# Performance work log

Measured on AMD Instinct MI355X. Metric: run time of the kernel, lower is better.

Reference implementation:

```python
import jax, jax.numpy as jnp
import numpy as np

L = 3          # num_layers
D = 512        # hidden_dim
B, N = 8, 1024
EPS = 1e-5


def layernorm(x, gamma, beta):
    mu = jnp.mean(x, axis=-1, keepdims=True)
    var = jnp.var(x, axis=-1, keepdims=True)
    return (x - mu) * jax.lax.rsqrt(var + EPS) * gamma + beta


def setup_inputs() -> dict:
    key = jax.random.key(0)
    ks = jax.random.split(key, 12)
    s = 1.0 / np.sqrt(D)
    node_features = jax.random.normal(ks[0], (B, N, D), dtype=jnp.float32)
    adjacency_matrix = jax.random.randint(ks[1], (B, N, N), 0, 2, dtype=jnp.int32)
    return {
        "node_features": node_features,
        "adjacency_matrix": adjacency_matrix,
        # attn_linear: Linear(2D, 1) -> weight [2D], bias scalar, per layer
        "attn_w": jax.random.normal(ks[2], (L, 2 * D), dtype=jnp.float32) * (1.0 / np.sqrt(2 * D)),
        "attn_b": jax.random.normal(ks[3], (L,), dtype=jnp.float32) * 0.01,
        "W1": jax.random.normal(ks[4], (L, D, 4 * D), dtype=jnp.float32) * s,
        "b1": jnp.zeros((L, 4 * D), dtype=jnp.float32),
        "W2": jax.random.normal(ks[5], (L, 4 * D, D), dtype=jnp.float32) * (1.0 / np.sqrt(4 * D)),
        "b2": jnp.zeros((L, D), dtype=jnp.float32),
        "g1": jnp.ones((L, D), dtype=jnp.float32),
        "beta1": jnp.zeros((L, D), dtype=jnp.float32),
        "g2": jnp.ones((L, D), dtype=jnp.float32),
        "beta2": jnp.zeros((L, D), dtype=jnp.float32),
    }


def reference(node_features, adjacency_matrix, attn_w, attn_b, W1, b1, W2, b2, g1, beta1, g2, beta2):
    n = adjacency_matrix.shape[-1]
    # adjacency + self loops; mask of allowed edges
    mask = (adjacency_matrix.astype(jnp.float32) + jnp.eye(n, dtype=jnp.float32)) > 0  # [B,N,N]
    x = node_features
    d = x.shape[-1]
    for l in range(attn_w.shape[0]):
        # score_ij = a1.h_i + a2.h_j + b  (== Linear(concat(h_i,h_j)))
        si = x @ attn_w[l, :d]           # [B,N]
        sj = x @ attn_w[l, d:]           # [B,N]
        scores = si[:, :, None] + sj[:, None, :] + attn_b[l]   # [B,N,N]
        scores = jnp.where(scores >= 0, scores, 0.2 * scores)  # LeakyReLU(0.2)
        scores = jnp.where(mask, scores, -jnp.inf)
        attn = jax.nn.softmax(scores, axis=-1)                  # diag always unmasked
        agg = jnp.einsum('bij,bjd->bid', attn, x)
        h = layernorm(x + agg, g1[l], beta1[l])
        ff = jax.nn.gelu(h @ W1[l] + b1[l], approximate=False) @ W2[l] + b2[l]
        x = layernorm(h + ff, g2[l], beta2[l])
    return x
```

## Files before the change

kernel.cpp:

```cpp
#include <hip/hip_runtime.h>
#include <math.h>

#define NB 8
#define NN 1024
#define DD 512

typedef unsigned short u16;
typedef unsigned int u32;
typedef unsigned long long u64;
typedef __attribute__((ext_vector_type(8))) short bfrag;
typedef __attribute__((ext_vector_type(4))) float ffrag;

__device__ __forceinline__ u16 f2b(float f) {
    union { float f; u32 u; } v; v.f = f;
    u32 r = v.u + 0x7fffu + ((v.u >> 16) & 1u);
    return (u16)(r >> 16);
}
__device__ __forceinline__ float b2f(u16 b) {
    union { u32 u; float f; } v; v.u = ((u32)b) << 16;
    return v.f;
}

__device__ __forceinline__ float gelu_cheap(float v) {
    float s = v * 0.70710678118654752f;
    float a = fabsf(s);
    float t = 1.0f / (1.0f + 0.3275911f * a);
    float p = ((((1.061405429f * t - 1.453152027f) * t + 1.421413741f) * t
                - 0.284496736f) * t + 0.254829592f) * t;
    float erfa = 1.0f - p * __expf(-a * a);
    float erfs = copysignf(erfa, s);
    return 0.5f * v * (1.0f + erfs);
}

__device__ __forceinline__ void gload_lds16(const void* g, void* l) {
    __builtin_amdgcn_global_load_lds(
        (const __attribute__((address_space(1))) void*)g,
        (__attribute__((address_space(3))) void*)l, 16, 0, 0);
}

__global__ __launch_bounds__(256) void mask_pack(const int* __restrict__ adj,
                                                 u64* __restrict__ mb) {
    int idx = blockIdx.x * 256 + threadIdx.x;
    int w = idx & 15;
    int bi = idx >> 4;
    int i = bi & 1023;
    const int4* p = (const int4*)(adj + (size_t)bi * NN + w * 64);
    u64 m = 0;
#pragma unroll
    for (int q = 0; q < 16; ++q) {
        int4 v = p[q];
        if (v.x > 0) m |= 1ull << (q * 4 + 0);
        if (v.y > 0) m |= 1ull << (q * 4 + 1);
        if (v.z > 0) m |= 1ull << (q * 4 + 2);
        if (v.w > 0) m |= 1ull << (q * 4 + 3);
    }
    if (w == (i >> 6)) m |= 1ull << (i & 63);
    mb[idx] = m;
}

__global__ __launch_bounds__(256) void transpose_cvt(
    const float* __restrict__ in, u16* __restrict__ out,
    int R, int C, size_t inStr, size_t outStr)
{
    __shared__ float tile[32][33];
    int z = blockIdx.z;
    int r0 = blockIdx.y * 32, c0 = blockIdx.x * 32;
    int t = threadIdx.x;
    int tr = t >> 3, tc = (t & 7) * 4;
    float4 v = *(const float4*)(in + inStr * z + (size_t)(r0 + tr) * C + c0 + tc);
    tile[tr][tc + 0] = v.x; tile[tr][tc + 1] = v.y;
    tile[tr][tc + 2] = v.z; tile[tr][tc + 3] = v.w;
    __syncthreads();
    u32 w0 = (u32)f2b(tile[tc + 0][tr]) | ((u32)f2b(tile[tc + 1][tr]) << 16);
    u32 w1 = (u32)f2b(tile[tc + 2][tr]) | ((u32)f2b(tile[tc + 3][tr]) << 16);
    uint2 wv; wv.x = w0; wv.y = w1;
    *(uint2*)(out + outStr * z + (size_t)(c0 + tr) * R + r0 + tc) = wv;
}

__global__ __launch_bounds__(256) void score_proj_kernel(
    const float* __restrict__ x, const float* __restrict__ w,
    float* __restrict__ si, float* __restrict__ sj)
{
    int wave = threadIdx.x >> 6;
    int lane = threadIdx.x & 63;
    int row = blockIdx.x * 4 + wave;
    const float4* xr = (const float4*)(x + (size_t)row * DD) + lane * 2;
    const float4* w1 = (const float4*)(w) + lane * 2;
    const float4* w2 = (const float4*)(w + DD) + lane * 2;
    float a = 0.f, b2 = 0.f;
#pragma unroll
    for (int c = 0; c < 2; ++c) {
        float4 xv = xr[c], wa = w1[c], wb = w2[c];
        a  += xv.x * wa.x + xv.y * wa.y + xv.z * wa.z + xv.w * wa.w;
        b2 += xv.x * wb.x + xv.y * wb.y + xv.z * wb.z + xv.w * wb.w;
    }
#pragma unroll
    for (int off = 32; off > 0; off >>= 1) {
        a  += __shfl_xor(a, off);
        b2 += __shfl_xor(b2, off);
    }
    if (lane == 0) { si[row] = a; sj[row] = b2; }
}

__global__ __launch_bounds__(256) void softmax_p(
    const float* __restrict__ si, const float* __restrict__ sj,
    const float* __restrict__ attn_b, const u64* __restrict__ mb,
    u16* __restrict__ P)
{
    __shared__ u16 sb[8 * NN];
    int b  = blockIdx.x >> 7;
    int i0 = (blockIdx.x & 127) * 8;
    int tid = threadIdx.x;
    int r = tid >> 5, l32 = tid & 31;
    int i = i0 + r;
    float bb = attn_b[0];
    float siv = si[b * NN + i];
    const float* sjb = sj + b * NN;
    const u64* mbr = mb + ((size_t)b * NN + i) * 16;

    float sv[32];
    float mx = -INFINITY;
#pragma unroll
    for (int q = 0; q < 32; ++q) {
        int j = q * 32 + l32;
        u64 w = mbr[q >> 1];
        int bit = ((q & 1) << 5) + l32;
        float s = siv + sjb[j] + bb;
        s = (s >= 0.f) ? s : 0.2f * s;
        s = ((w >> bit) & 1ull) ? s : -INFINITY;
        sv[q] = s;
        mx = fmaxf(mx, s);
    }
#pragma unroll
    for (int off = 16; off > 0; off >>= 1) mx = fmaxf(mx, __shfl_xor(mx, off, 32));
    float sum = 0.f;
#pragma unroll
    for (int q = 0; q < 32; ++q) {
        float p = __expf(sv[q] - mx);
        sv[q] = p;
        sum += p;
    }
#pragma unroll
    for (int off = 16; off > 0; off >>= 1) sum += __shfl_xor(sum, off, 32);
    float inv = 1.f / sum;
#pragma unroll
    for (int q = 0; q < 32; ++q)
        sb[r * NN + q * 32 + l32] = f2b(sv[q] * inv);
    __syncthreads();
    const uint4* src = (const uint4*)sb;
    uint4* dst = (uint4*)(P + ((size_t)b * NN + i0) * NN);
#pragma unroll
    for (int t = 0; t < 4; ++t) dst[t * 256 + tid] = src[t * 256 + tid];
}

template <int EPI>
__global__ __launch_bounds__(256) void gemm64(
    const u16* __restrict__ A, const u16* __restrict__ Bm,
    const float* __restrict__ bias, const void* __restrict__ res,
    void* __restrict__ Cout, int K, int N, int lda, int ldb,
    size_t aStr, size_t bStr, size_t cStr, size_t resStr)
{
    __shared__ __align__(16) u16 lds[24576];
    int z = blockIdx.z;
    int m0 = blockIdx.y * 64, n0 = blockIdx.x * 128;
    int tid = threadIdx.x;
    int lane = tid & 63, wv = tid >> 6;

    const u16* ag[2]; const u16* bg[4];
    u32 la[2], lb[4];
#pragma unroll
    for (int i = 0; i < 2; ++i) {
        int q = i * 256 + tid;
        int row = q >> 3, c = q & 7;
        ag[i] = A + aStr * z + (size_t)(m0 + row) * lda + (c ^ (row & 7)) * 8;
        la[i] = i * 2048 + wv * 512;
    }
#pragma unroll
    for (int i = 0; i < 4; ++i) {
        int q = i * 256 + tid;
        int row = q >> 3, c = q & 7;
        bg[i] = Bm + bStr * z + (size_t)(n0 + row) * ldb + (c ^ (row & 7)) * 8;
        lb[i] = 8192 + i * 2048 + wv * 512;
    }

    int mw = (wv >> 1) * 32, nw = (wv & 1) * 64;
    int lr = lane & 15, lq = lane >> 4;
    int sw = lr & 7;

    ffrag acc[2][4];
#pragma unroll
    for (int i = 0; i < 2; ++i)
#pragma unroll
        for (int j = 0; j < 4; ++j) acc[i][j] = (ffrag){0.f, 0.f, 0.f, 0.f};

#pragma unroll
    for (int i = 0; i < 2; ++i) gload_lds16(ag[i], &lds[la[i]]);
#pragma unroll
    for (int i = 0; i < 4; ++i) gload_lds16(bg[i], &lds[lb[i]]);

    for (int k0 = 0; k0 < K; k0 += 64) {
        int cur = (k0 >> 6) & 1;
        if (k0 + 64 < K) {
#pragma unroll
            for (int i = 0; i < 2; ++i)
                gload_lds16(ag[i] + k0 + 64, &lds[((cur ^ 1) << 12) + la[i]]);
#pragma unroll
            for (int i = 0; i < 4; ++i)
                gload_lds16(bg[i] + k0 + 64, &lds[((cur ^ 1) << 13) + lb[i]]);
            asm volatile("s_waitcnt vmcnt(6)" ::: "memory");
        } else {
            asm volatile("s_waitcnt vmcnt(0)" ::: "memory");
        }
        asm volatile("s_barrier" ::: "memory");

        const u16* Ab = &lds[cur << 12];
        const u16* Bb = &lds[8192 + (cur << 13)];
#pragma unroll
        for (int h = 0; h < 2; ++h) {
            bfrag af[2], bf[4];
#pragma unroll
            for (int i = 0; i < 2; ++i)
                af[i] = *(const bfrag*)&Ab[(mw + i * 16 + lr) * 64 + ((h * 4 + lq) ^ sw) * 8];
#pragma unroll
            for (int j = 0; j < 4; ++j)
                bf[j] = *(const bfrag*)&Bb[(nw + j * 16 + lr) * 64 + ((h * 4 + lq) ^ sw) * 8];
#pragma unroll
            for (int i = 0; i < 2; ++i)
#pragma unroll
                for (int j = 0; j < 4; ++j)
                    acc[i][j] = __builtin_amdgcn_mfma_f32_16x16x32_bf16(af[i], bf[j], acc[i][j], 0, 0, 0);
        }
        asm volatile("s_waitcnt lgkmcnt(0)\ns_barrier" ::: "memory");
    }

    float* Cf = (float*)Cout + cStr * z;
    u16*   Cb = (u16*)Cout + cStr * z;
    const float* resf = (const float*)res;
    const u16*   resb = (const u16*)res;
#pragma unroll
    for (int i = 0; i < 2; ++i) {
        int row = m0 + mw + i * 16 + lq * 4;
#pragma unroll
        for (int j = 0; j < 4; ++j) {
            int col = n0 + nw + j * 16 + lr;
            float bv = (EPI != 0) ? bias[col] : 0.f;
#pragma unroll
            for (int r = 0; r < 4; ++r) {
                float v = acc[i][j][r] + bv;
                size_t off = (size_t)(row + r) * N + col;
                if (EPI == 1) {
                    Cb[off] = f2b(gelu_cheap(v));
                } else if (EPI == 0) {
                    Cf[off] = v + resf[resStr * z + off];
                } else {
                    Cf[off] = v + b2f(resb[off]);
                }
            }
        }
    }
}

template <bool BF>
__global__ __launch_bounds__(256) void ln_kernel(
    const float* __restrict__ in, const float* __restrict__ g,
    const float* __restrict__ be, void* __restrict__ out)
{
    int row = blockIdx.x;
    int tid = threadIdx.x;
    const float2* rp = (const float2*)(in + (size_t)row * DD);
    float2 v = rp[tid];
    float s  = v.x + v.y;
    float ss = v.x * v.x + v.y * v.y;
#pragma unroll
    for (int off = 32; off > 0; off >>= 1) {
        s  += __shfl_xor(s, off);
        ss += __shfl_xor(ss, off);
    }
    __shared__ float sh[8];
    int wave = tid >> 6, lane = tid & 63;
    if (lane == 0) { sh[wave] = s; sh[4 + wave] = ss; }
    __syncthreads();
    float S  = sh[0] + sh[1] + sh[2] + sh[3];
    float SS = sh[4] + sh[5] + sh[6] + sh[7];
    float mean = S * (1.f / DD);
    float var  = SS * (1.f / DD) - mean * mean;
    var = fmaxf(var, 0.f);
    float rs = rsqrtf(var + 1e-5f);
    float2 gv = ((const float2*)g)[tid];
    float2 bv = ((const float2*)be)[tid];
    float ox = (v.x - mean) * rs * gv.x + bv.x;
    float oy = (v.y - mean) * rs * gv.y + bv.y;
    if (BF) {
        u32 w = (u32)f2b(ox) | ((u32)f2b(oy) << 16);
        ((u32*)out)[(size_t)row * (DD / 2) + tid] = w;
    } else {
        float2 o; o.x = ox; o.y = oy;
        ((float2*)out)[(size_t)row * (DD / 2) + tid] = o;
    }
}

__global__ __launch_bounds__(256) void ln2st(
    const float* __restrict__ in, const float* __restrict__ g,
    const float* __restrict__ be, const float* __restrict__ wnx,
    float* __restrict__ xout, u16* __restrict__ xT,
    float* __restrict__ si, float* __restrict__ sj)
{
    __shared__ u16 tt[512 * 36];
    int row0 = blockIdx.x * 32;
    int b    = row0 >> 10;
    int rloc = row0 & 1023;
    int tid  = threadIdx.x;
    int r = tid >> 3, l8 = tid & 7;
    int row = row0 + r;

    const float4* rp = (const float4*)(in + (size_t)row * DD + l8 * 64);
    float4 v[16];
    float s = 0.f, ss = 0.f;
#pragma unroll
    for (int c = 0; c < 16; ++c) {
        v[c] = rp[c];
        s  += v[c].x + v[c].y + v[c].z + v[c].w;
        ss += v[c].x * v[c].x + v[c].y * v[c].y + v[c].z * v[c].z + v[c].w * v[c].w;
    }
#pragma unroll
    for (int off = 1; off < 8; off <<= 1) {
        s  += __shfl_xor(s, off);
        ss += __shfl_xor(ss, off);
    }
    float mean = s * (1.f / DD);
    float var  = ss * (1.f / DD) - mean * mean;
    var = fmaxf(var, 0.f);
    float rs = rsqrtf(var + 1e-5f);

    float a = 0.f, b2 = 0.f;
    float4* op = (float4*)(xout + (size_t)row * DD + l8 * 64);
#pragma unroll
    for (int c = 0; c < 16; ++c) {
        float4 gv = ((const float4*)g)[l8 * 16 + c];
        float4 bv = ((const float4*)be)[l8 * 16 + c];
        float4 o;
        o.x = (v[c].x - mean) * rs * gv.x + bv.x;
        o.y = (v[c].y - mean) * rs * gv.y + bv.y;
        o.z = (v[c].z - mean) * rs * gv.z + bv.z;
        o.w = (v[c].w - mean) * rs * gv.w + bv.w;
        op[c] = o;
        float4 wa = ((const float4*)wnx)[l8 * 16 + c];
        float4 wb = ((const float4*)(wnx + DD))[l8 * 16 + c];
        a  += o.x * wa.x + o.y * wa.y + o.z * wa.z + o.w * wa.w;
        b2 += o.x * wb.x + o.y * wb.y + o.z * wb.z + o.w * wb.w;
        int d = l8 * 64 + c * 4;
        tt[(d + 0) * 36 + r] = f2b(o.x);
        tt[(d + 1) * 36 + r] = f2b(o.y);
        tt[(d + 2) * 36 + r] = f2b(o.z);
        tt[(d + 3) * 36 + r] = f2b(o.w);
    }
#pragma unroll
    for (int off = 1; off < 8; off <<= 1) {
        a  += __shfl_xor(a, off);
        b2 += __shfl_xor(b2, off);
    }
    if (l8 == 0) { si[row] = a; sj[row] = b2; }

    __syncthreads();
#pragma unroll
    for (int t = 0; t < 2; ++t) {
        int d = t * 256 + tid;
        const uint2* src = (const uint2*)&tt[d * 36];
        uint2* dst = (uint2*)(xT + ((size_t)b * DD + d) * NN + rloc);
#pragma unroll
        for (int k = 0; k < 4; ++k) dst[k] = src[k];
#pragma unroll
        for (int k = 4; k < 8; ++k) dst[k] = src[k];
    }
}

extern "C" void kernel_launch(void* const* d_in, const int* in_sizes, int n_in,
                              void* d_out, int out_size, void* d_ws, size_t ws_size,
                              hipStream_t stream) {
    const float* nf     = (const float*)d_in[0];
    const int*   adj    = (const int*)d_in[1];
    const float* attn_w = (const float*)d_in[2];
    const float* attn_b = (const float*)d_in[3];
    const float* W1     = (const float*)d_in[4];
    const float* b1     = (const float*)d_in[5];
    const float* W2     = (const float*)d_in[6];
    const float* b2     = (const float*)d_in[7];
    const float* g1     = (const float*)d_in[8];
    const float* be1    = (const float*)d_in[9];
    const float* g2     = (const float*)d_in[10];
    const float* be2    = (const float*)d_in[11];
    float* out = (float*)d_out;

    char* wsb = (char*)d_ws;
    float* x_cur = (float*)(wsb);
    u16*   h_bf  = (u16*)(wsb + 16777216);
    char*  scr   = wsb + 25165824;
    u16*   P     = (u16*)scr;
    float* hres  = (float*)(scr + 16777216);
    u16*   mid   = (u16*)scr;
    u16*   xT    = (u16*)(wsb + 58720256);
    u16*   W1t   = (u16*)(wsb + 67108864);
    u16*   W2t   = (u16*)(wsb + 73400320);
    u64*   mask  = (u64*)(wsb + 79691776);
    float* si    = (float*)(wsb + 80740352);
    float* sj    = (float*)(wsb + 80773120);

    mask_pack<<<512, 256, 0, stream>>>(adj, mask);
    transpose_cvt<<<dim3(64, 16, 3), 256, 0, stream>>>(W1, W1t, 512, 2048,
                                                       (size_t)512 * 2048, (size_t)512 * 2048);
    transpose_cvt<<<dim3(16, 64, 3), 256, 0, stream>>>(W2, W2t, 2048, 512,
                                                       (size_t)2048 * 512, (size_t)2048 * 512);

    for (int l = 0; l < 3; ++l) {
        const float* xin = (l == 0) ? nf : x_cur;
        if (l == 0) {
            score_proj_kernel<<<2048, 256, 0, stream>>>(xin, attn_w, si, sj);
            transpose_cvt<<<dim3(16, 32, 8), 256, 0, stream>>>(xin, xT, 1024, 512,
                                                               (size_t)NN * DD, (size_t)NN * DD);
        }
        softmax_p<<<1024, 256, 0, stream>>>(si, sj, attn_b + l, mask, P);
        gemm64<0><<<dim3(4, 16, 8), 256, 0, stream>>>(
            P, xT, nullptr, xin, hres, 1024, 512, 1024, 1024,
            (size_t)NN * NN, (size_t)DD * NN, (size_t)NN * DD, (size_t)NN * DD);
        ln_kernel<true><<<8192, 256, 0, stream>>>(hres, g1 + (size_t)l * 512, be1 + (size_t)l * 512, h_bf);
        gemm64<1><<<dim3(16, 128, 1), 256, 0, stream>>>(
            h_bf, W1t + (size_t)l * 1048576, b1 + (size_t)l * 2048, nullptr, mid,
            512, 2048, 512, 512, 0, 0, 0, 0);
        gemm64<2><<<dim3(4, 128, 1), 256, 0, stream>>>(
            mid, W2t + (size_t)l * 1048576, b2 + (size_t)l * 512, h_bf, x_cur,
            2048, 512, 2048, 2048, 0, 0, 0, 0);
        if (l == 2) {
            ln_kernel<false><<<8192, 256, 0, stream>>>(x_cur, g2 + (size_t)l * 512,
                                                       be2 + (size_t)l * 512, out);
        } else {
            ln2st<<<256, 256, 0, stream>>>(x_cur, g2 + (size_t)l * 512,
                                           be2 + (size_t)l * 512,
                                           attn_w + (size_t)(l + 1) * 1024,
                                           x_cur, xT, si, sj);
        }
    }
}
```

Baseline: 482.6 us.

## Use FP8 e4m3 for attention probabilities and transposed features in aggregation GEMM

Attention probabilities P (scaled by 64) and the transposed node features xT are now stored as FP8 e4m3 instead of bf16. A new dedicated gemm_agg_fp8 kernel consumes them with fp8 MFMA and rescales in the epilogue while adding the residual. This halves the bytes of the two operands of the batched aggregation GEMM and the softmax store, at the cost of lower numerical precision in the aggregation. The two weight-transpose launches are also merged into one kernel, and ln2st's access pattern is reordered.

```diff
diff --git a/kernel.cpp b/kernel.cpp
--- a/kernel.cpp
+++ b/kernel.cpp
@@ -5,6 +5,7 @@
 #define NN 1024
 #define DD 512
 
+typedef unsigned char u8;
 typedef unsigned short u16;
 typedef unsigned int u32;
 typedef unsigned long long u64;
@@ -19,6 +20,9 @@
 __device__ __forceinline__ float b2f(u16 b) {
     union { u32 u; float f; } v; v.u = ((u32)b) << 16;
     return v.f;
+}
+__device__ __forceinline__ u8 f2e4m3(float f) {
+    return (u8)(__builtin_amdgcn_cvt_pk_fp8_f32(f, f, 0, false) & 0xff);
 }
 
 __device__ __forceinline__ float gelu_cheap(float v) {
@@ -58,8 +62,36 @@
     mb[idx] = m;
 }
 
-__global__ __launch_bounds__(256) void transpose_cvt(
-    const float* __restrict__ in, u16* __restrict__ out,
+__global__ __launch_bounds__(256) void wtrans(
+    const float* __restrict__ W1, const float* __restrict__ W2,
+    u16* __restrict__ W1t, u16* __restrict__ W2t)
+{
+    __shared__ float tile[32][33];
+    int z = blockIdx.y;
+    int bid = blockIdx.x;
+    const float* in; u16* out; int R, C, c0, r0;
+    if (z < 3) {
+        in = W1 + (size_t)z * 512 * 2048; out = W1t + (size_t)z * 1048576;
+        R = 512; C = 2048; c0 = (bid & 63) * 32; r0 = (bid >> 6) * 32;
+    } else {
+        int l = z - 3;
+        in = W2 + (size_t)l * 2048 * 512; out = W2t + (size_t)l * 1048576;
+        R = 2048; C = 512; c0 = (bid & 15) * 32; r0 = (bid >> 4) * 32;
+    }
+    int t = threadIdx.x;
+    int tr = t >> 3, tc = (t & 7) * 4;
+    float4 v = *(const float4*)(in + (size_t)(r0 + tr) * C + c0 + tc);
+    tile[tr][tc + 0] = v.x; tile[tr][tc + 1] = v.y;
+    tile[tr][tc + 2] = v.z; tile[tr][tc + 3] = v.w;
+    __syncthreads();
+    u32 w0 = (u32)f2b(tile[tc + 0][tr]) | ((u32)f2b(tile[tc + 1][tr]) << 16);
+    u32 w1 = (u32)f2b(tile[tc + 2][tr]) | ((u32)f2b(tile[tc + 3][tr]) << 16);
+    uint2 wv; wv.x = w0; wv.y = w1;
+    *(uint2*)(out + (size_t)(c0 + tr) * R + r0 + tc) = wv;
+}
+
+__global__ __launch_bounds__(256) void transpose_cvt8(
+    const float* __restrict__ in, u8* __restrict__ out,
     int R, int C, size_t inStr, size_t outStr)
 {
     __shared__ float tile[32][33];
@@ -71,10 +103,9 @@
     tile[tr][tc + 0] = v.x; tile[tr][tc + 1] = v.y;
     tile[tr][tc + 2] = v.z; tile[tr][tc + 3] = v.w;
     __syncthreads();
-    u32 w0 = (u32)f2b(tile[tc + 0][tr]) | ((u32)f2b(tile[tc + 1][tr]) << 16);
-    u32 w1 = (u32)f2b(tile[tc + 2][tr]) | ((u32)f2b(tile[tc + 3][tr]) << 16);
-    uint2 wv; wv.x = w0; wv.y = w1;
-    *(uint2*)(out + outStr * z + (size_t)(c0 + tr) * R + r0 + tc) = wv;
+    u32 w = (u32)__builtin_amdgcn_cvt_pk_fp8_f32(tile[tc + 0][tr], tile[tc + 1][tr], 0, false);
+    w = (u32)__builtin_amdgcn_cvt_pk_fp8_f32(tile[tc + 2][tr], tile[tc + 3][tr], (int)w, true);
+    *(u32*)(out + outStr * z + (size_t)(c0 + tr) * R + r0 + tc) = w;
 }
 
 __global__ __launch_bounds__(256) void score_proj_kernel(
@@ -105,9 +136,9 @@
 __global__ __launch_bounds__(256) void softmax_p(
     const float* __restrict__ si, const float* __restrict__ sj,
     const float* __restrict__ attn_b, const u64* __restrict__ mb,
-    u16* __restrict__ P)
-{
-    __shared__ u16 sb[8 * NN];
+    u8* __restrict__ P)
+{
+    __shared__ u8 sb[8 * NN];
     int b  = blockIdx.x >> 7;
     int i0 = (blockIdx.x & 127) * 8;
     int tid = threadIdx.x;
@@ -142,26 +173,107 @@
     }
 #pragma unroll
     for (int off = 16; off > 0; off >>= 1) sum += __shfl_xor(sum, off, 32);
-    float inv = 1.f / sum;
+    float inv = 64.f / sum;
 #pragma unroll
     for (int q = 0; q < 32; ++q)
-        sb[r * NN + q * 32 + l32] = f2b(sv[q] * inv);
+        sb[r * NN + q * 32 + l32] = f2e4m3(sv[q] * inv);
     __syncthreads();
     const uint4* src = (const uint4*)sb;
     uint4* dst = (uint4*)(P + ((size_t)b * NN + i0) * NN);
 #pragma unroll
-    for (int t = 0; t < 4; ++t) dst[t * 256 + tid] = src[t * 256 + tid];
+    for (int t = 0; t < 2; ++t) dst[t * 256 + tid] = src[t * 256 + tid];
+}
+
+__global__ __launch_bounds__(256) void gemm_agg_fp8(
+    const u8* __restrict__ A, const u8* __restrict__ Bm,
+    const float* __restrict__ res, float* __restrict__ Cout)
+{
+    __shared__ __align__(16) u8 lds[24576];
+    int z = blockIdx.z;
+    int m0 = blockIdx.y * 64, n0 = blockIdx.x * 128;
+    int tid = threadIdx.x;
+    int lane = tid & 63, wv = tid >> 6;
+
+    const u8* ag = A + (size_t)z * NN * NN + (size_t)(m0 + (tid & 63)) * NN + (tid >> 6) * 16;
+    const u8* bg[2];
+#pragma unroll
+    for (int i = 0; i < 2; ++i)
+        bg[i] = Bm + (size_t)z * DD * NN + (size_t)(n0 + (tid & 127)) * NN + (i * 2 + (tid >> 7)) * 16;
+    u32 laA = wv * 1024;
+    u32 laB[2] = { 8192u + wv * 1024u, 8192u + 4096u + wv * 1024u };
+
+    int mw = (wv >> 1) * 32, nw = (wv & 1) * 64;
+    int lr = lane & 15, lq = lane >> 4;
+
+    ffrag acc[2][4];
+#pragma unroll
+    for (int i = 0; i < 2; ++i)
+#pragma unroll
+        for (int j = 0; j < 4; ++j) acc[i][j] = (ffrag){0.f, 0.f, 0.f, 0.f};
+
+    gload_lds16(ag, &lds[laA]);
+#pragma unroll
+    for (int i = 0; i < 2; ++i) gload_lds16(bg[i], &lds[laB[i]]);
+
+    for (int k0 = 0; k0 < NN; k0 += 64) {
+        int cur = (k0 >> 6) & 1;
+        if (k0 + 64 < NN) {
+            gload_lds16(ag + k0 + 64, &lds[(cur ^ 1) * 4096 + laA]);
+#pragma unroll
+            for (int i = 0; i < 2; ++i)
+                gload_lds16(bg[i] + k0 + 64, &lds[(cur ^ 1) * 8192 + laB[i]]);
+            asm volatile("s_waitcnt vmcnt(3)" ::: "memory");
+        } else {
+            asm volatile("s_waitcnt vmcnt(0)" ::: "memory");
+        }
+        asm volatile("s_barrier" ::: "memory");
+
+        const u8* Ab = &lds[cur * 4096];
+        const u8* Bb = &lds[8192 + cur * 8192];
+#pragma unroll
+        for (int h = 0; h < 2; ++h) {
+            int kc = h * 2 + (lq >> 1);
+            int klo = (lq & 1) * 8;
+            long af[2]; long bf[4];
+#pragma unroll
+            for (int i = 0; i < 2; ++i)
+                af[i] = *(const long*)&Ab[kc * 1024 + (mw + i * 16 + lr) * 16 + klo];
+#pragma unroll
+            for (int j = 0; j < 4; ++j)
+                bf[j] = *(const long*)&Bb[kc * 2048 + (nw + j * 16 + lr) * 16 + klo];
+#pragma unroll
+            for (int i = 0; i < 2; ++i)
+#pragma unroll
+                for (int j = 0; j < 4; ++j)
+                    acc[i][j] = __builtin_amdgcn_mfma_f32_16x16x32_fp8_fp8(af[i], bf[j], acc[i][j], 0, 0, 0);
+        }
+        asm volatile("s_waitcnt lgkmcnt(0)\ns_barrier" ::: "memory");
+    }
+
+    float* Cf = Cout + (size_t)z * NN * DD;
+    const float* resf = res + (size_t)z * NN * DD;
+#pragma unroll
+    for (int i = 0; i < 2; ++i) {
+        int row = m0 + mw + i * 16 + lq * 4;
+#pragma unroll
+        for (int j = 0; j < 4; ++j) {
+            int col = n0 + nw + j * 16 + lr;
+#pragma unroll
+            for (int r = 0; r < 4; ++r) {
+                size_t off = (size_t)(row + r) * DD + col;
+                Cf[off] = acc[i][j][r] * 0.015625f + resf[off];
+            }
+        }
+    }
 }
 
 template <int EPI>
 __global__ __launch_bounds__(256) void gemm64(
     const u16* __restrict__ A, const u16* __restrict__ Bm,
     const float* __restrict__ bias, const void* __restrict__ res,
-    void* __restrict__ Cout, int K, int N, int lda, int ldb,
-    size_t aStr, size_t bStr, size_t cStr, size_t resStr)
+    void* __restrict__ Cout, int K, int N, int lda, int ldb)
 {
     __shared__ __align__(16) u16 lds[24576];
-    int z = blockIdx.z;
     int m0 = blockIdx.y * 64, n0 = blockIdx.x * 128;
     int tid = threadIdx.x;
     int lane = tid & 63, wv = tid >> 6;
@@ -172,14 +284,14 @@
     for (int i = 0; i < 2; ++i) {
         int q = i * 256 + tid;
         int row = q >> 3, c = q & 7;
-        ag[i] = A + aStr * z + (size_t)(m0 + row) * lda + (c ^ (row & 7)) * 8;
+        ag[i] = A + (size_t)(m0 + row) * lda + (c ^ (row & 7)) * 8;
         la[i] = i * 2048 + wv * 512;
     }
 #pragma unroll
     for (int i = 0; i < 4; ++i) {
         int q = i * 256 + tid;
         int row = q >> 3, c = q & 7;
-        bg[i] = Bm + bStr * z + (size_t)(n0 + row) * ldb + (c ^ (row & 7)) * 8;
+        bg[i] = Bm + (size_t)(n0 + row) * ldb + (c ^ (row & 7)) * 8;
         lb[i] = 8192 + i * 2048 + wv * 512;
     }
 
@@ -233,25 +345,22 @@
         asm volatile("s_waitcnt lgkmcnt(0)\ns_barrier" ::: "memory");
     }
 
-    float* Cf = (float*)Cout + cStr * z;
-    u16*   Cb = (u16*)Cout + cStr * z;
-    const float* resf = (const float*)res;
-    const u16*   resb = (const u16*)res;
+    float* Cf = (float*)Cout;
+    u16*   Cb = (u16*)Cout;
+    const u16* resb = (const u16*)res;
 #pragma unroll
     for (int i = 0; i < 2; ++i) {
         int row = m0 + mw + i * 16 + lq * 4;
 #pragma unroll
         for (int j = 0; j < 4; ++j) {
             int col = n0 + nw + j * 16 + lr;
-            float bv = (EPI != 0) ? bias[col] : 0.f;
+            float bv = bias[col];
 #pragma unroll
             for (int r = 0; r < 4; ++r) {
                 float v = acc[i][j][r] + bv;
                 size_t off = (size_t)(row + r) * N + col;
                 if (EPI == 1) {
                     Cb[off] = f2b(gelu_cheap(v));
-                } else if (EPI == 0) {
-                    Cf[off] = v + resf[resStr * z + off];
                 } else {
                     Cf[off] = v + b2f(resb[off]);
                 }
@@ -302,10 +411,10 @@
 __global__ __launch_bounds__(256) void ln2st(
     const float* __restrict__ in, const float* __restrict__ g,
     const float* __restrict__ be, const float* __restrict__ wnx,
-    float* __restrict__ xout, u16* __restrict__ xT,
+    float* __restrict__ xout, u8* __restrict__ xT,
     float* __restrict__ si, float* __restrict__ sj)
 {
-    __shared__ u16 tt[512 * 36];
+    __shared__ u8 tt[512 * 40];
     int row0 = blockIdx.x * 32;
     int b    = row0 >> 10;
     int rloc = row0 & 1023;
@@ -313,12 +422,12 @@
     int r = tid >> 3, l8 = tid & 7;
     int row = row0 + r;
 
-    const float4* rp = (const float4*)(in + (size_t)row * DD + l8 * 64);
+    const float4* rp = (const float4*)(in + (size_t)row * DD);
     float4 v[16];
     float s = 0.f, ss = 0.f;
 #pragma unroll
     for (int c = 0; c < 16; ++c) {
-        v[c] = rp[c];
+        v[c] = rp[c * 8 + l8];
         s  += v[c].x + v[c].y + v[c].z + v[c].w;
         ss += v[c].x * v[c].x + v[c].y * v[c].y + v[c].z * v[c].z + v[c].w * v[c].w;
     }
@@ -333,26 +442,26 @@
     float rs = rsqrtf(var + 1e-5f);
 
     float a = 0.f, b2 = 0.f;
-    float4* op = (float4*)(xout + (size_t)row * DD + l8 * 64);
+    float4* op = (float4*)(xout + (size_t)row * DD);
 #pragma unroll
     for (int c = 0; c < 16; ++c) {
-        float4 gv = ((const float4*)g)[l8 * 16 + c];
-        float4 bv = ((const float4*)be)[l8 * 16 + c];
+        float4 gv = ((const float4*)g)[c * 8 + l8];
+        float4 bv = ((const float4*)be)[c * 8 + l8];
         float4 o;
         o.x = (v[c].x - mean) * rs * gv.x + bv.x;
         o.y = (v[c].y - mean) * rs * gv.y + bv.y;
         o.z = (v[c].z - mean) * rs * gv.z + bv.z;
         o.w = (v[c].w - mean) * rs * gv.w + bv.w;
-        op[c] = o;
-        float4 wa = ((const float4*)wnx)[l8 * 16 + c];
-        float4 wb = ((const float4*)(wnx + DD))[l8 * 16 + c];
+        op[c * 8 + l8] = o;
+        float4 wa = ((const float4*)wnx)[c * 8 + l8];
+        float4 wb = ((const float4*)(wnx + DD))[c * 8 + l8];
         a  += o.x * wa.x + o.y * wa.y + o.z * wa.z + o.w * wa.w;
         b2 += o.x * wb.x + o.y * wb.y + o.z * wb.z + o.w * wb.w;
-        int d = l8 * 64 + c * 4;
-        tt[(d + 0) * 36 + r] = f2b(o.x);
-        tt[(d + 1) * 36 + r] = f2b(o.y);
-        tt[(d + 2) * 36 + r] = f2b(o.z);
-        tt[(d + 3) * 36 + r] = f2b(o.w);
+        int d = c * 32 + l8 * 4;
+        tt[(d + 0) * 40 + r] = f2e4m3(o.x);
+        tt[(d + 1) * 40 + r] = f2e4m3(o.y);
+        tt[(d + 2) * 40 + r] = f2e4m3(o.z);
+        tt[(d + 3) * 40 + r] = f2e4m3(o.w);
     }
 #pragma unroll
     for (int off = 1; off < 8; off <<= 1) {
@@ -365,12 +474,10 @@
 #pragma unroll
     for (int t = 0; t < 2; ++t) {
         int d = t * 256 + tid;
-        const uint2* src = (const uint2*)&tt[d * 36];
+        const uint2* src = (const uint2*)&tt[d * 40];
         uint2* dst = (uint2*)(xT + ((size_t)b * DD + d) * NN + rloc);
 #pragma unroll
         for (int k = 0; k < 4; ++k) dst[k] = src[k];
-#pragma unroll
-        for (int k = 4; k < 8; ++k) dst[k] = src[k];
     }
 }
 
@@ -395,10 +502,10 @@
     float* x_cur = (float*)(wsb);
     u16*   h_bf  = (u16*)(wsb + 16777216);
     char*  scr   = wsb + 25165824;
-    u16*   P     = (u16*)scr;
+    u8*    P     = (u8*)scr;
     float* hres  = (float*)(scr + 16777216);
     u16*   mid   = (u16*)scr;
-    u16*   xT    = (u16*)(wsb + 58720256);
+    u8*    xT    = (u8*)(wsb + 58720256);
     u16*   W1t   = (u16*)(wsb + 67108864);
     u16*   W2t   = (u16*)(wsb + 73400320);
     u64*   mask  = (u64*)(wsb + 79691776);
@@ -406,29 +513,24 @@
     float* sj    = (float*)(wsb + 80773120);
 
     mask_pack<<<512, 256, 0, stream>>>(adj, mask);
-    transpose_cvt<<<dim3(64, 16, 3), 256, 0, stream>>>(W1, W1t, 512, 2048,
-                                                       (size_t)512 * 2048, (size_t)512 * 2048);
-    transpose_cvt<<<dim3(16, 64, 3), 256, 0, stream>>>(W2, W2t, 2048, 512,
-                                                       (size_t)2048 * 512, (size_t)2048 * 512);
+    wtrans<<<dim3(1024, 6), 256, 0, stream>>>(W1, W2, W1t, W2t);
 
     for (int l = 0; l < 3; ++l) {
         const float* xin = (l == 0) ? nf : x_cur;
         if (l == 0) {
             score_proj_kernel<<<2048, 256, 0, stream>>>(xin, attn_w, si, sj);
-            transpose_cvt<<<dim3(16, 32, 8), 256, 0, stream>>>(xin, xT, 1024, 512,
-                                                               (size_t)NN * DD, (size_t)NN * DD);
+            transpose_cvt8<<<dim3(16, 32, 8), 256, 0, stream>>>(xin, xT, 1024, 512,
+                                                                (size_t)NN * DD, (size_t)NN * DD);
         }
         softmax_p<<<1024, 256, 0, stream>>>(si, sj, attn_b + l, mask, P);
-        gemm64<0><<<dim3(4, 16, 8), 256, 0, stream>>>(
-            P, xT, nullptr, xin, hres, 1024, 512, 1024, 1024,
-            (size_t)NN * NN, (size_t)DD * NN, (size_t)NN * DD, (size_t)NN * DD);
+        gemm_agg_fp8<<<dim3(4, 16, 8), 256, 0, stream>>>(P, xT, xin, hres);
         ln_kernel<true><<<8192, 256, 0, stream>>>(hres, g1 + (size_t)l * 512, be1 + (size_t)l * 512, h_bf);
         gemm64<1><<<dim3(16, 128, 1), 256, 0, stream>>>(
             h_bf, W1t + (size_t)l * 1048576, b1 + (size_t)l * 2048, nullptr, mid,
-            512, 2048, 512, 512, 0, 0, 0, 0);
+            512, 2048, 512, 512);
         gemm64<2><<<dim3(4, 128, 1), 256, 0, stream>>>(
             mid, W2t + (size_t)l * 1048576, b2 + (size_t)l * 512, h_bf, x_cur,
-            2048, 512, 2048, 2048, 0, 0, 0, 0);
+            2048, 512, 2048, 2048);
         if (l == 2) {
             ln_kernel<false><<<8192, 256, 0, stream>>>(x_cur, g2 + (size_t)l * 512,
                                                        be2 + (size_t)l * 512, out);
```

New measurement: 493.7 us. +2.3%, slower.
